# Performance work log

Measured on AMD Instinct MI355X. Metric: run time of the kernel, lower is better.

Reference implementation:

```python
import jax, jax.numpy as jnp
import numpy as np

STATE_DIM = 128
HIDDEN = 128
NUM_HEADS = 16
TEMPERATURE = 1.0
NEG_INF = float('-inf')


def setup_inputs() -> dict:
    key = jax.random.key(0)
    ks = jax.random.split(key, 8)
    B, S = 2, 512
    state_embeddings = jax.random.normal(ks[0], (B, S, STATE_DIM), dtype=jnp.float32)
    mask = jnp.ones((B, S, S), dtype=bool)
    # MLP params (Linear stores [in, out] here; we apply x @ W + b)
    W1 = jax.random.normal(ks[1], (2 * STATE_DIM, HIDDEN), dtype=jnp.float32) / np.sqrt(2 * STATE_DIM)
    b1 = jnp.zeros((HIDDEN,), dtype=jnp.float32)
    W2 = jax.random.normal(ks[2], (HIDDEN, HIDDEN), dtype=jnp.float32) / np.sqrt(HIDDEN)
    b2 = jnp.zeros((HIDDEN,), dtype=jnp.float32)
    W3 = jax.random.normal(ks[3], (HIDDEN, NUM_HEADS), dtype=jnp.float32) / np.sqrt(HIDDEN)
    b3 = jnp.zeros((NUM_HEADS,), dtype=jnp.float32)
    head_temperatures = jnp.ones((NUM_HEADS,), dtype=jnp.float32) * TEMPERATURE
    return {
        'state_embeddings': state_embeddings,
        'mask': mask,
        'W1': W1, 'b1': b1, 'W2': W2, 'b2': b2, 'W3': W3, 'b3': b3,
        'head_temperatures': head_temperatures,
    }


def reference(state_embeddings, mask, W1, b1, W2, b2, W3, b3, head_temperatures):
    # Split first Linear: cat([x_i, x_j]) @ W1 == x_i @ W1a + x_j @ W1b
    # This avoids materializing the [B, S, S, 2*state_dim] pairwise concat
    # while computing identical math.
    W1a, W1b = W1[:STATE_DIM], W1[STATE_DIM:]
    hi = jnp.einsum('bsd,dh->bsh', state_embeddings, W1a) + b1  # [B,S,H]
    hj = jnp.einsum('bsd,dh->bsh', state_embeddings, W1b)       # [B,S,H]
    h = jax.nn.relu(hi[:, :, None, :] + hj[:, None, :, :])       # [B,S,S,H]
    h = jax.nn.relu(jnp.einsum('bijh,hk->bijk', h, W2) + b2)     # [B,S,S,H]
    comp = jnp.einsum('bijh,hn->bijn', h, W3) + b3               # [B,S,S,heads]
    bias = jnp.transpose(comp, (0, 3, 1, 2))                     # [B,heads,S,S]
    bias = bias * head_temperatures[None, :, None, None]
    bias = jnp.where(mask[:, None, :, :], bias, NEG_INF)
    return bias
```

## Files before the change

kernel.cpp:

```cpp
#include <hip/hip_runtime.h>
#include <math.h>

typedef _Float16 half8 __attribute__((ext_vector_type(8)));
typedef _Float16 half4v __attribute__((ext_vector_type(4)));
typedef float floatx4 __attribute__((ext_vector_type(4)));

__global__ __launch_bounds__(256) void prep_kernel(
    const float* __restrict__ E,
    const float* __restrict__ W1,
    const float* __restrict__ b1,
    const float* __restrict__ W2,
    const float* __restrict__ W3,
    _Float16* __restrict__ hih,
    _Float16* __restrict__ hjh,
    _Float16* __restrict__ W2frag,
    _Float16* __restrict__ W3frag)
{
    const int blk = blockIdx.x;
    const int t = threadIdx.x;
    if (blk < 1024) {
        __shared__ float sE[128];
        if (t < 128) sE[t] = E[blk*128 + t];
        __syncthreads();
        const int half = t >> 7;
        const int k = t & 127;
        float acc = half ? 0.f : b1[k];
        const float* w1col = &W1[half*128*128 + k];
        #pragma unroll 8
        for (int d = 0; d < 128; ++d)
            acc = fmaf(sE[d], w1col[d*128], acc);
        if (half == 0) hih[blk*128 + k] = (_Float16)acc;
        else           hjh[blk*128 + k] = (_Float16)acc;
    } else if (blk == 1024) {
        for (int e = t; e < 16384; e += 256) {
            int q = e & 7, l = (e >> 3) & 63, g = e >> 9;
            int wr = g >> 4, nt = (g >> 2) & 3, ks = g & 3;
            int row = 64*wr + 16*nt + (l & 15);
            int k = ks*32 + (l >> 4)*8 + q;
            W2frag[e] = (_Float16)W2[k*128 + row];
        }
    } else {
        for (int e = t; e < 2048; e += 256) {
            int q = e & 7, l = (e >> 3) & 63, ks = e >> 9;
            int k = ks*32 + (l >> 4)*8 + q;
            W3frag[e] = (_Float16)W3[k*16 + (l & 15)];
        }
    }
}

__global__ __launch_bounds__(256, 3) void main_kernel(
    const _Float16* __restrict__ hih,
    const _Float16* __restrict__ hjh,
    const _Float16* __restrict__ W2frag,
    const _Float16* __restrict__ W3frag,
    const float* __restrict__ b2,
    const float* __restrict__ b3,
    const float* __restrict__ temps,
    const int* __restrict__ mask,
    float* __restrict__ out)
{
    constexpr int PADH = 136;
    __shared__ _Float16 sH[128 * PADH];

    const int tid = threadIdx.x;
    const int bid = blockIdx.x;
    const int b  = bid >> 11;
    const int i  = (bid >> 2) & 511;
    const int j0 = (bid & 3) << 7;

    const int lane = tid & 63;
    const int wave = tid >> 6;
    const int wr = wave >> 1;
    const int wc = wave & 1;
    const int lr = lane & 15;
    const int lq = lane >> 4;

    const half8 zero8 = {};
    const _Float16* hirow = &hih[(b*512 + i)*128];
    const _Float16* hjbase = &hjh[(b*512 + j0)*128];
    const half8* w2v = (const half8*)W2frag;

    half8 aW[4][4];
    #pragma unroll
    for (int nt = 0; nt < 4; ++nt)
        #pragma unroll
        for (int ks = 0; ks < 4; ++ks)
            aW[nt][ks] = w2v[((wr*4 + nt)*4 + ks)*64 + lane];

    half8 hiF[4];
    #pragma unroll
    for (int ks = 0; ks < 4; ++ks)
        hiF[ks] = *(const half8*)&hirow[ks*32 + lq*8];

    #pragma unroll
    for (int kk = 0; kk < 8; ++kk) {
        const int c = kk*256 + tid;
        const int row = c >> 4, col = c & 15;
        half8 v = *(const half8*)&hjbase[row*128 + col*8];
        *(half8*)&sH[row*PADH + col*8] = v;
    }
    __syncthreads();

    floatx4 acc[4][4] = {};
    #pragma unroll
    for (int ks = 0; ks < 4; ++ks) {
        const int kb = ks*32 + lq*8;
        half8 bF[4];
        #pragma unroll
        for (int mt = 0; mt < 4; ++mt) {
            const int m = 64*wc + 16*mt + lr;
            half8 hj8 = *(const half8*)&sH[m*PADH + kb];
            bF[mt] = __builtin_elementwise_max(hiF[ks] + hj8, zero8);
        }
        #pragma unroll
        for (int nt = 0; nt < 4; ++nt)
            #pragma unroll
            for (int mt = 0; mt < 4; ++mt)
                acc[nt][mt] = __builtin_amdgcn_mfma_f32_16x16x32_f16(
                    aW[nt][ks], bF[mt], acc[nt][mt], 0, 0, 0);
    }
    __syncthreads();

    #pragma unroll
    for (int nt = 0; nt < 4; ++nt) {
        const int nb = 64*wr + 16*nt + 4*lq;
        const float4 bv = *(const float4*)&b2[nb];
        #pragma unroll
        for (int mt = 0; mt < 4; ++mt) {
            const int m = 64*wc + 16*mt + lr;
            floatx4 v = acc[nt][mt];
            half4v o;
            o[0] = (_Float16)fmaxf(v[0] + bv.x, 0.f);
            o[1] = (_Float16)fmaxf(v[1] + bv.y, 0.f);
            o[2] = (_Float16)fmaxf(v[2] + bv.z, 0.f);
            o[3] = (_Float16)fmaxf(v[3] + bv.w, 0.f);
            *(half4v*)&sH[m*PADH + nb] = o;
        }
    }

    const int* mrow = &mask[(b*512 + i)*512];
    const int m0 = 32*wave;
    int4 mk0 = *(const int4*)&mrow[j0 + m0 + 4*lq];
    int4 mk1 = *(const int4*)&mrow[j0 + m0 + 16 + 4*lq];
    __syncthreads();

    const half8* w3v = (const half8*)W3frag;
    floatx4 acc2[2] = {};
    #pragma unroll
    for (int ks = 0; ks < 4; ++ks) {
        const int k0 = ks*32 + lq*8;
        half8 bW = w3v[ks*64 + lane];
        half8 a0 = *(const half8*)&sH[(m0 + lr)*PADH + k0];
        half8 a1 = *(const half8*)&sH[(m0 + 16 + lr)*PADH + k0];
        acc2[0] = __builtin_amdgcn_mfma_f32_16x16x32_f16(a0, bW, acc2[0], 0, 0, 0);
        acc2[1] = __builtin_amdgcn_mfma_f32_16x16x32_f16(a1, bW, acc2[1], 0, 0, 0);
    }

    const int n2 = lr;
    const float tempv = temps[n2];
    const float b3v = b3[n2];
    float* outp = &out[(((b*16 + n2)*512) + i)*512];
    {
        const int j = j0 + m0 + 4*lq;
        floatx4 v = acc2[0];
        float4 res;
        res.x = mk0.x ? (v[0] + b3v)*tempv : -INFINITY;
        res.y = mk0.y ? (v[1] + b3v)*tempv : -INFINITY;
        res.z = mk0.z ? (v[2] + b3v)*tempv : -INFINITY;
        res.w = mk0.w ? (v[3] + b3v)*tempv : -INFINITY;
        *(float4*)&outp[j] = res;
    }
    {
        const int j = j0 + m0 + 16 + 4*lq;
        floatx4 v = acc2[1];
        float4 res;
        res.x = mk1.x ? (v[0] + b3v)*tempv : -INFINITY;
        res.y = mk1.y ? (v[1] + b3v)*tempv : -INFINITY;
        res.z = mk1.z ? (v[2] + b3v)*tempv : -INFINITY;
        res.w = mk1.w ? (v[3] + b3v)*tempv : -INFINITY;
        *(float4*)&outp[j] = res;
    }
}

extern "C" void kernel_launch(void* const* d_in, const int* in_sizes, int n_in,
                              void* d_out, int out_size, void* d_ws, size_t ws_size,
                              hipStream_t stream)
{
    const float* E     = (const float*)d_in[0];
    const int* mask    = (const int*)d_in[1];
    const float* W1    = (const float*)d_in[2];
    const float* b1    = (const float*)d_in[3];
    const float* W2    = (const float*)d_in[4];
    const float* b2    = (const float*)d_in[5];
    const float* W3    = (const float*)d_in[6];
    const float* b3    = (const float*)d_in[7];
    const float* temps = (const float*)d_in[8];

    char* ws = (char*)d_ws;
    _Float16* hih = (_Float16*)ws;
    _Float16* hjh = (_Float16*)(ws + 262144);
    _Float16* W2f = (_Float16*)(ws + 524288);
    _Float16* W3f = W2f + 16384;

    prep_kernel<<<1026, 256, 0, stream>>>(E, W1, b1, W2, W3, hih, hjh, W2f, W3f);
    main_kernel<<<4096, 256, 0, stream>>>(hih, hjh, W2f, W3f, b2, b3, temps, mask,
                                          (float*)d_out);
}
```

Baseline: 116.1 us.

## Process four query rows per block, reusing staged hj tile and weights

Each main-kernel block now loops over four i rows and reuses the shared-memory hj tile, the W2/W3 fragments and the biases loaded once, instead of reloading them per row. Shared memory uses an XOR swizzle instead of padding, with a separate buffer for the second-layer activations, and outputs go through nontemporal stores. The prep kernel computes four embedding rows per block so each W1 load is shared. This cuts grid size and redundant loads at the cost of lower occupancy (launch bounds 2) and less parallelism per block.

```diff
diff --git a/kernel.cpp b/kernel.cpp
--- a/kernel.cpp
+++ b/kernel.cpp
@@ -18,20 +18,31 @@
 {
     const int blk = blockIdx.x;
     const int t = threadIdx.x;
-    if (blk < 1024) {
-        __shared__ float sE[128];
-        if (t < 128) sE[t] = E[blk*128 + t];
+    if (blk < 256) {
+        __shared__ float sE[4][128];
+        const int r0 = blk * 4;
+        for (int e = t; e < 512; e += 256)
+            sE[e >> 7][e & 127] = E[r0*128 + e];
         __syncthreads();
         const int half = t >> 7;
         const int k = t & 127;
-        float acc = half ? 0.f : b1[k];
+        float a0 = half ? 0.f : b1[k];
+        float a1 = a0, a2 = a0, a3 = a0;
         const float* w1col = &W1[half*128*128 + k];
         #pragma unroll 8
-        for (int d = 0; d < 128; ++d)
-            acc = fmaf(sE[d], w1col[d*128], acc);
-        if (half == 0) hih[blk*128 + k] = (_Float16)acc;
-        else           hjh[blk*128 + k] = (_Float16)acc;
-    } else if (blk == 1024) {
+        for (int d = 0; d < 128; ++d) {
+            const float w = w1col[d*128];
+            a0 = fmaf(sE[0][d], w, a0);
+            a1 = fmaf(sE[1][d], w, a1);
+            a2 = fmaf(sE[2][d], w, a2);
+            a3 = fmaf(sE[3][d], w, a3);
+        }
+        _Float16* dst = half ? hjh : hih;
+        dst[(r0+0)*128 + k] = (_Float16)a0;
+        dst[(r0+1)*128 + k] = (_Float16)a1;
+        dst[(r0+2)*128 + k] = (_Float16)a2;
+        dst[(r0+3)*128 + k] = (_Float16)a3;
+    } else if (blk == 256) {
         for (int e = t; e < 16384; e += 256) {
             int q = e & 7, l = (e >> 3) & 63, g = e >> 9;
             int wr = g >> 4, nt = (g >> 2) & 3, ks = g & 3;
@@ -48,7 +59,11 @@
     }
 }
 
-__global__ __launch_bounds__(256, 3) void main_kernel(
+__device__ __forceinline__ int swz(int row, int chunk) {
+    return row*128 + ((chunk ^ (row & 7)) << 3);
+}
+
+__global__ __launch_bounds__(256, 2) void main_kernel(
     const _Float16* __restrict__ hih,
     const _Float16* __restrict__ hjh,
     const _Float16* __restrict__ W2frag,
@@ -59,13 +74,13 @@
     const int* __restrict__ mask,
     float* __restrict__ out)
 {
-    constexpr int PADH = 136;
-    __shared__ _Float16 sH[128 * PADH];
+    __shared__ __align__(16) _Float16 sHJ[128 * 128];
+    __shared__ __align__(16) _Float16 sH2[128 * 128];
 
     const int tid = threadIdx.x;
     const int bid = blockIdx.x;
-    const int b  = bid >> 11;
-    const int i  = (bid >> 2) & 511;
+    const int b  = bid >> 9;
+    const int i0 = ((bid >> 2) & 127) << 2;
     const int j0 = (bid & 3) << 7;
 
     const int lane = tid & 63;
@@ -74,11 +89,13 @@
     const int wc = wave & 1;
     const int lr = lane & 15;
     const int lq = lane >> 4;
+    const int m0 = 32*wave;
 
     const half8 zero8 = {};
-    const _Float16* hirow = &hih[(b*512 + i)*128];
+    const _Float16* hirow = &hih[(b*512 + i0)*128];
     const _Float16* hjbase = &hjh[(b*512 + j0)*128];
     const half8* w2v = (const half8*)W2frag;
+    const half8* w3v = (const half8*)W3frag;
 
     half8 aW[4][4];
     #pragma unroll
@@ -87,98 +104,114 @@
         for (int ks = 0; ks < 4; ++ks)
             aW[nt][ks] = w2v[((wr*4 + nt)*4 + ks)*64 + lane];
 
+    half8 w3F[4];
+    #pragma unroll
+    for (int ks = 0; ks < 4; ++ks)
+        w3F[ks] = w3v[ks*64 + lane];
+
+    float4 bv[4];
+    #pragma unroll
+    for (int nt = 0; nt < 4; ++nt)
+        bv[nt] = *(const float4*)&b2[64*wr + 16*nt + 4*lq];
+
     half8 hiF[4];
     #pragma unroll
     for (int ks = 0; ks < 4; ++ks)
         hiF[ks] = *(const half8*)&hirow[ks*32 + lq*8];
+
+    const int n2 = lr;
+    const float tempv = temps[n2];
+    const float b3v = b3[n2];
 
     #pragma unroll
     for (int kk = 0; kk < 8; ++kk) {
         const int c = kk*256 + tid;
         const int row = c >> 4, col = c & 15;
         half8 v = *(const half8*)&hjbase[row*128 + col*8];
-        *(half8*)&sH[row*PADH + col*8] = v;
+        *(half8*)&sHJ[swz(row, col)] = v;
     }
     __syncthreads();
 
-    floatx4 acc[4][4] = {};
-    #pragma unroll
-    for (int ks = 0; ks < 4; ++ks) {
-        const int kb = ks*32 + lq*8;
-        half8 bF[4];
-        #pragma unroll
-        for (int mt = 0; mt < 4; ++mt) {
-            const int m = 64*wc + 16*mt + lr;
-            half8 hj8 = *(const half8*)&sH[m*PADH + kb];
-            bF[mt] = __builtin_elementwise_max(hiF[ks] + hj8, zero8);
-        }
-        #pragma unroll
-        for (int nt = 0; nt < 4; ++nt)
-            #pragma unroll
-            for (int mt = 0; mt < 4; ++mt)
-                acc[nt][mt] = __builtin_amdgcn_mfma_f32_16x16x32_f16(
-                    aW[nt][ks], bF[mt], acc[nt][mt], 0, 0, 0);
-    }
-    __syncthreads();
-
-    #pragma unroll
-    for (int nt = 0; nt < 4; ++nt) {
-        const int nb = 64*wr + 16*nt + 4*lq;
-        const float4 bv = *(const float4*)&b2[nb];
-        #pragma unroll
-        for (int mt = 0; mt < 4; ++mt) {
-            const int m = 64*wc + 16*mt + lr;
-            floatx4 v = acc[nt][mt];
-            half4v o;
-            o[0] = (_Float16)fmaxf(v[0] + bv.x, 0.f);
-            o[1] = (_Float16)fmaxf(v[1] + bv.y, 0.f);
-            o[2] = (_Float16)fmaxf(v[2] + bv.z, 0.f);
-            o[3] = (_Float16)fmaxf(v[3] + bv.w, 0.f);
-            *(half4v*)&sH[m*PADH + nb] = o;
-        }
-    }
-
-    const int* mrow = &mask[(b*512 + i)*512];
-    const int m0 = 32*wave;
-    int4 mk0 = *(const int4*)&mrow[j0 + m0 + 4*lq];
-    int4 mk1 = *(const int4*)&mrow[j0 + m0 + 16 + 4*lq];
-    __syncthreads();
-
-    const half8* w3v = (const half8*)W3frag;
-    floatx4 acc2[2] = {};
-    #pragma unroll
-    for (int ks = 0; ks < 4; ++ks) {
-        const int k0 = ks*32 + lq*8;
-        half8 bW = w3v[ks*64 + lane];
-        half8 a0 = *(const half8*)&sH[(m0 + lr)*PADH + k0];
-        half8 a1 = *(const half8*)&sH[(m0 + 16 + lr)*PADH + k0];
-        acc2[0] = __builtin_amdgcn_mfma_f32_16x16x32_f16(a0, bW, acc2[0], 0, 0, 0);
-        acc2[1] = __builtin_amdgcn_mfma_f32_16x16x32_f16(a1, bW, acc2[1], 0, 0, 0);
-    }
-
-    const int n2 = lr;
-    const float tempv = temps[n2];
-    const float b3v = b3[n2];
-    float* outp = &out[(((b*16 + n2)*512) + i)*512];
-    {
-        const int j = j0 + m0 + 4*lq;
-        floatx4 v = acc2[0];
-        float4 res;
-        res.x = mk0.x ? (v[0] + b3v)*tempv : -INFINITY;
-        res.y = mk0.y ? (v[1] + b3v)*tempv : -INFINITY;
-        res.z = mk0.z ? (v[2] + b3v)*tempv : -INFINITY;
-        res.w = mk0.w ? (v[3] + b3v)*tempv : -INFINITY;
-        *(float4*)&outp[j] = res;
-    }
-    {
-        const int j = j0 + m0 + 16 + 4*lq;
-        floatx4 v = acc2[1];
-        float4 res;
-        res.x = mk1.x ? (v[0] + b3v)*tempv : -INFINITY;
-        res.y = mk1.y ? (v[1] + b3v)*tempv : -INFINITY;
-        res.z = mk1.z ? (v[2] + b3v)*tempv : -INFINITY;
-        res.w = mk1.w ? (v[3] + b3v)*tempv : -INFINITY;
-        *(float4*)&outp[j] = res;
+    for (int ii = 0; ii < 4; ++ii) {
+        const int i = i0 + ii;
+
+        floatx4 acc[4][4] = {};
+        #pragma unroll
+        for (int ks = 0; ks < 4; ++ks) {
+            half8 bF[4];
+            #pragma unroll
+            for (int mt = 0; mt < 4; ++mt) {
+                const int m = 64*wc + 16*mt + lr;
+                half8 hj8 = *(const half8*)&sHJ[swz(m, ks*4 + lq)];
+                bF[mt] = __builtin_elementwise_max(hiF[ks] + hj8, zero8);
+            }
+            #pragma unroll
+            for (int nt = 0; nt < 4; ++nt)
+                #pragma unroll
+                for (int mt = 0; mt < 4; ++mt)
+                    acc[nt][mt] = __builtin_amdgcn_mfma_f32_16x16x32_f16(
+                        aW[nt][ks], bF[mt], acc[nt][mt], 0, 0, 0);
+        }
+
+        {
+            const _Float16* hin = &hirow[((ii < 3) ? (ii + 1) : ii)*128];
+            #pragma unroll
+            for (int ks = 0; ks < 4; ++ks)
+                hiF[ks] = *(const half8*)&hin[ks*32 + lq*8];
+        }
+
+        #pragma unroll
+        for (int nt = 0; nt < 4; ++nt) {
+            const int nb = 64*wr + 16*nt + 4*lq;
+            #pragma unroll
+            for (int mt = 0; mt < 4; ++mt) {
+                const int m = 64*wc + 16*mt + lr;
+                floatx4 v = acc[nt][mt];
+                half4v o;
+                o[0] = (_Float16)fmaxf(v[0] + bv[nt].x, 0.f);
+                o[1] = (_Float16)fmaxf(v[1] + bv[nt].y, 0.f);
+                o[2] = (_Float16)fmaxf(v[2] + bv[nt].z, 0.f);
+                o[3] = (_Float16)fmaxf(v[3] + bv[nt].w, 0.f);
+                *(half4v*)&sH2[swz(m, nb >> 3) + (nb & 7)] = o;
+            }
+        }
+
+        const int* mrow = &mask[(b*512 + i)*512];
+        int4 mk0 = *(const int4*)&mrow[j0 + m0 + 4*lq];
+        int4 mk1 = *(const int4*)&mrow[j0 + m0 + 16 + 4*lq];
+        __syncthreads();
+
+        floatx4 acc2[2] = {};
+        #pragma unroll
+        for (int ks = 0; ks < 4; ++ks) {
+            half8 a0v = *(const half8*)&sH2[swz(m0 + lr, ks*4 + lq)];
+            half8 a1v = *(const half8*)&sH2[swz(m0 + 16 + lr, ks*4 + lq)];
+            acc2[0] = __builtin_amdgcn_mfma_f32_16x16x32_f16(a0v, w3F[ks], acc2[0], 0, 0, 0);
+            acc2[1] = __builtin_amdgcn_mfma_f32_16x16x32_f16(a1v, w3F[ks], acc2[1], 0, 0, 0);
+        }
+
+        float* outp = &out[(((b*16 + n2)*512) + i)*512];
+        {
+            const int j = j0 + m0 + 4*lq;
+            floatx4 v = acc2[0];
+            floatx4 res;
+            res[0] = mk0.x ? (v[0] + b3v)*tempv : -INFINITY;
+            res[1] = mk0.y ? (v[1] + b3v)*tempv : -INFINITY;
+            res[2] = mk0.z ? (v[2] + b3v)*tempv : -INFINITY;
+            res[3] = mk0.w ? (v[3] + b3v)*tempv : -INFINITY;
+            __builtin_nontemporal_store(res, (floatx4*)&outp[j]);
+        }
+        {
+            const int j = j0 + m0 + 16 + 4*lq;
+            floatx4 v = acc2[1];
+            floatx4 res;
+            res[0] = mk1.x ? (v[0] + b3v)*tempv : -INFINITY;
+            res[1] = mk1.y ? (v[1] + b3v)*tempv : -INFINITY;
+            res[2] = mk1.z ? (v[2] + b3v)*tempv : -INFINITY;
+            res[3] = mk1.w ? (v[3] + b3v)*tempv : -INFINITY;
+            __builtin_nontemporal_store(res, (floatx4*)&outp[j]);
+        }
+        __syncthreads();
     }
 }
 
@@ -202,7 +235,7 @@
     _Float16* W2f = (_Float16*)(ws + 524288);
     _Float16* W3f = W2f + 16384;
 
-    prep_kernel<<<1026, 256, 0, stream>>>(E, W1, b1, W2, W3, hih, hjh, W2f, W3f);
-    main_kernel<<<4096, 256, 0, stream>>>(hih, hjh, W2f, W3f, b2, b3, temps, mask,
+    prep_kernel<<<258, 256, 0, stream>>>(E, W1, b1, W2, W3, hih, hjh, W2f, W3f);
+    main_kernel<<<1024, 256, 0, stream>>>(hih, hjh, W2f, W3f, b2, b3, temps, mask,
                                           (float*)d_out);
 }
```

Result: faster. 113.7 us (-2.1%).
